# Optimization experiments

Hardware: AMD Instinct MI355X
Metric: run time of the kernel (lower is better)

Reference implementation:

```python
import jax, jax.numpy as jnp
import numpy as np

SEQ = 4096
R_DIM = 1024
Z_DIM = 1024
AT_DIM = 1024
G_DIM = 1024


def _xavier(key, shape):
    fan_in, fan_out = shape[1], shape[0]
    limit = float(np.sqrt(6.0 / (fan_in + fan_out)))
    return jax.random.uniform(key, shape, jnp.float32, -limit, limit)


def setup_inputs() -> dict:
    key = jax.random.key(0)
    ks = jax.random.split(key, 12)
    return {
        "R": jax.random.normal(ks[0], (SEQ, R_DIM), jnp.float32),
        "W_alpha": _xavier(ks[1], (R_DIM, 2 * R_DIM)),
        "b_alpha": jnp.zeros((R_DIM,), jnp.float32),
        "W_delta": _xavier(ks[2], (R_DIM, 2 * R_DIM)),
        "b_delta": jnp.zeros((R_DIM,), jnp.float32),
        "W_q": _xavier(ks[3], (AT_DIM, Z_DIM)),
        "b_q": jnp.zeros((AT_DIM,), jnp.float32),
        "W_k": _xavier(ks[4], (AT_DIM, Z_DIM)),
        "b_k": jnp.zeros((AT_DIM,), jnp.float32),
        "W_v": _xavier(ks[5], (AT_DIM, Z_DIM)),
        "b_v": jnp.zeros((AT_DIM,), jnp.float32),
        "W_z": _xavier(ks[6], (Z_DIM, R_DIM)),
        "b_z": jnp.zeros((Z_DIM,), jnp.float32),
        "W_f": _xavier(ks[7], (AT_DIM, G_DIM)),
        "b_f": jnp.zeros((AT_DIM,), jnp.float32),
        "W_EMA": _xavier(ks[8], (G_DIM, R_DIM)),
        "b_EMA": jnp.zeros((G_DIM,), jnp.float32),
        "W_z_at": _xavier(ks[9], (G_DIM, AT_DIM)),
        "b_z_at": jnp.zeros((G_DIM,), jnp.float32),
        "W_i": _xavier(ks[10], (1, R_DIM)),
        "b_i": jnp.zeros((1,), jnp.float32),
        "W_final": _xavier(ks[11], (1, G_DIM)),
    }


def reference(R, W_alpha, b_alpha, W_delta, b_delta, W_q, b_q, W_k, b_k,
              W_v, b_v, W_z, b_z, W_f, b_f, W_EMA, b_EMA, W_z_at, b_z_at,
              W_i, b_i, W_final):
    r_dim = R.shape[-1]
    at_dim = W_q.shape[0]
    # prepend zero row; r_t / r_{t-1} pairs
    R2 = jnp.concatenate([jnp.zeros((1, r_dim), R.dtype), R], axis=0)
    r_t, r_prev = R2[1:], R2[:-1]
    concat_r = jnp.concatenate([r_prev, r_t], axis=1)  # [m, 2r]
    alpha = jnp.tanh(concat_r @ W_alpha.T + b_alpha)
    delta = jnp.tanh(concat_r @ W_delta.T + b_delta)
    R_EMA = alpha * r_t + (1.0 - alpha) * delta * r_prev
    Z = jax.nn.silu(R_EMA @ W_z.T + b_z)
    Q = Z @ W_q.T + b_q
    K = Z @ W_k.T + b_k
    V = Z @ W_v.T + b_v
    scores = (Q @ K.T) / jnp.sqrt(jnp.float32(at_dim))  # [m, m]
    weights = jax.nn.softmax(scores, axis=-1)
    Z_at = weights @ V
    R_EMA_p = R_EMA @ W_EMA.T + b_EMA
    f = jax.nn.sigmoid(R_EMA_p @ W_f.T + b_f)
    Z_at_p = f * Z_at
    Z_EMA_f = Z_at_p @ W_z_at.T + b_z_at
    Z_tp = jnp.tanh(R_EMA_p + Z_EMA_f)
    i = jnp.tanh(R_EMA @ W_i.T + b_i)  # [m, 1]
    Z_final = i * Z_tp + (1.0 - i) * R_EMA_p
    p_hat = jax.nn.sigmoid(Z_final @ W_final.T)  # [m, 1]
    return p_hat
```

## Files before the change

kernel.cpp:

```cpp
#include <hip/hip_runtime.h>
#include <cstdint>
#include <cmath>

#define MB (1024ull * 1024ull)

typedef unsigned short u16;
typedef __attribute__((ext_vector_type(8))) short short8;
typedef __attribute__((ext_vector_type(4))) float f32x4;

enum { M_TANH = 0, M_ZRE = 1, M_QKVF = 2, M_SCALE = 3, M_PVRAW = 4, M_F32 = 5 };

__device__ __forceinline__ u16 f2b(float f) {
  union { float f; uint32_t u; } v; v.f = f;
  uint32_t r = v.u + 0x7FFFu + ((v.u >> 16) & 1u);
  return (u16)(r >> 16);
}
__device__ __forceinline__ float b2f(u16 u) {
  union { uint32_t u; float f; } v; v.u = ((uint32_t)u) << 16;
  return v.f;
}

typedef __attribute__((address_space(3))) uint32_t lds_u32;
typedef const __attribute__((address_space(1))) uint32_t glb_u32;

__device__ __forceinline__ void gload16(const void* g, void* l) {
  __builtin_amdgcn_global_load_lds((glb_u32*)g, (lds_u32*)l, 16, 0, 0);
}

template <int MODE, int BNT>
__global__ __launch_bounds__(256) void gemm(const u16* __restrict__ A,
                                            const u16* __restrict__ B,
                                            const float* __restrict__ bias,
                                            const u16* __restrict__ A2,
                                            const u16* __restrict__ B2,
                                            const float* __restrict__ bias2,
                                            u16* __restrict__ Cb,
                                            u16* __restrict__ Cb2,
                                            u16* __restrict__ Cb3,
                                            float* __restrict__ Cf,
                                            int K, int lda, int ldb, float scale) {
  constexpr int NI = 4;
  constexpr int NJ = (BNT == 128) ? 4 : 2;
  __shared__ u16 As[2][128 * 32];
  __shared__ u16 Bs[2][BNT * 32];
  const int tid = threadIdx.x;
  const int wid = tid >> 6, lane = tid & 63;

  const int gx = gridDim.x, nwg = gx * gridDim.y;
  int id = blockIdx.y * gx + blockIdx.x;
  if ((nwg & 7) == 0) id = (id & 7) * (nwg >> 3) + (id >> 3);
  const int bm = (id / gx) * 128, bn = (id % gx) * BNT;
  const int wm = wid >> 1, wn = wid & 1;
  const int rowbase = wm * 64, colbase = wn * (BNT / 2);

  const bool isf = (MODE == M_QKVF) && (bn >= 3072);
  const u16* Ab = isf ? A2 : A;
  const u16* Bb = isf ? B2 : B;
  const int bnl = isf ? bn - 3072 : bn;
  const int kofs = (MODE == M_PVRAW) ? (int)blockIdx.z * K : 0;

  const int srow = tid >> 2;
  const int schunk = (tid & 3) ^ ((srow >> 1) & 3);
  const u16* gA = Ab + (size_t)(bm + srow) * lda + kofs + schunk * 8;
  const u16* gB = Bb + (size_t)(bnl + srow) * ldb + kofs + schunk * 8;

  f32x4 acc[NI][NJ];
#pragma unroll
  for (int i = 0; i < NI; ++i)
#pragma unroll
    for (int j = 0; j < NJ; ++j) acc[i][j] = (f32x4){0.f, 0.f, 0.f, 0.f};

  const int ar = lane & 15;
  const int pch = (((lane >> 4) ^ ((ar >> 1) & 3))) * 8;

  const int NT = K >> 5;

  auto stage = [&](int buf, int t) {
    const u16* a = gA + (size_t)t * 32;
    const u16* b = gB + (size_t)t * 32;
    gload16(a, &As[buf][wid * 512]);
    gload16(a + (size_t)64 * lda, &As[buf][wid * 512 + 2048]);
    gload16(b, &Bs[buf][wid * 512]);
    if (BNT == 128) gload16(b + (size_t)64 * ldb, &Bs[buf][wid * 512 + 2048]);
  };

  stage(0, 0);
  __syncthreads();
  int cur = 0;
  for (int t = 0; t < NT; ++t) {
    if (t + 1 < NT) stage(cur ^ 1, t + 1);
    short8 af[NI], bf[NJ];
#pragma unroll
    for (int i = 0; i < NI; ++i)
      af[i] = *reinterpret_cast<const short8*>(&As[cur][(rowbase + i * 16 + ar) * 32 + pch]);
#pragma unroll
    for (int j = 0; j < NJ; ++j)
      bf[j] = *reinterpret_cast<const short8*>(&Bs[cur][(colbase + j * 16 + ar) * 32 + pch]);
    __builtin_amdgcn_s_setprio(1);
#pragma unroll
    for (int i = 0; i < NI; ++i)
#pragma unroll
      for (int j = 0; j < NJ; ++j)
        acc[i][j] = __builtin_amdgcn_mfma_f32_16x16x32_bf16(af[i], bf[j], acc[i][j], 0, 0, 0);
    __builtin_amdgcn_s_setprio(0);
    __syncthreads();
    cur ^= 1;
  }

  float* Cfz = Cf;
  if (MODE == M_PVRAW && blockIdx.z != 0) Cfz = (float*)Cb3;

#pragma unroll
  for (int i = 0; i < NI; ++i) {
    const int rb = bm + rowbase + i * 16 + (lane >> 4) * 4;
#pragma unroll
    for (int j = 0; j < NJ; ++j) {
      const int n = bn + colbase + j * 16 + (lane & 15);
#pragma unroll
      for (int r = 0; r < 4; ++r) {
        const int m = rb + r;
        float v = acc[i][j][r];
        if (MODE == M_TANH) {
          v = tanhf(v + bias[n]);
          Cb[(size_t)m * 2048 + n] = f2b(v);
        } else if (MODE == M_ZRE) {
          v += bias[n];
          if (n < 1024) { const float s = v / (1.f + expf(-v)); Cb[(size_t)m * 1024 + n] = f2b(s); }
          else Cb2[(size_t)m * 1024 + (n - 1024)] = f2b(v);
        } else if (MODE == M_QKVF) {
          if (isf) {
            const int nl = n - 3072;
            const float s = 1.f / (1.f + expf(-(v + bias2[nl])));
            Cb3[(size_t)m * 1024 + nl] = f2b(s);
          } else {
            v += bias[n];
            if (n < 2048) Cb[(size_t)m * 2048 + n] = f2b(v);
            else Cb2[(size_t)m * 1024 + (n - 2048)] = f2b(v);
          }
        } else if (MODE == M_SCALE) {
          Cb[(size_t)m * 4096 + n] = f2b(v * scale);
        } else if (MODE == M_PVRAW) {
          Cfz[(size_t)m * 1024 + n] = v;
        } else if (MODE == M_F32) {
          Cf[(size_t)m * 1024 + n] = v + bias[n];
        }
      }
    }
  }
}

__global__ __launch_bounds__(256) void pv_reduce(const float* __restrict__ p0,
                                                 const float* __restrict__ p1,
                                                 const u16* __restrict__ fvb,
                                                 u16* __restrict__ Zatp) {
  const int idx = blockIdx.x * 256 + threadIdx.x;
  const float4 a = reinterpret_cast<const float4*>(p0)[idx];
  const float4 b = reinterpret_cast<const float4*>(p1)[idx];
  const ushort4 f4 = reinterpret_cast<const ushort4*>(fvb)[idx];
  ushort4 o;
  o.x = f2b((a.x + b.x) * b2f(f4.x));
  o.y = f2b((a.y + b.y) * b2f(f4.y));
  o.z = f2b((a.z + b.z) * b2f(f4.z));
  o.w = f2b((a.w + b.w) * b2f(f4.w));
  reinterpret_cast<ushort4*>(Zatp)[idx] = o;
}

__global__ __launch_bounds__(256) void convert_all(
    const float* __restrict__ s0, const float* __restrict__ s1, const float* __restrict__ s2,
    const float* __restrict__ s3, const float* __restrict__ s4, const float* __restrict__ s5,
    const float* __restrict__ s6, const float* __restrict__ s7, const float* __restrict__ s8,
    u16* __restrict__ Wad, u16* __restrict__ Wze, u16* __restrict__ Wqkv,
    u16* __restrict__ Wfb, u16* __restrict__ Wzab) {
  const int idx = blockIdx.x * 256 + threadIdx.x;
  const float* src; u16* dst; int off;
  if      (idx < 524288)  { src = s0; dst = Wad;           off = idx; }
  else if (idx < 1048576) { src = s1; dst = Wad + 2097152; off = idx - 524288; }
  else if (idx < 1310720) { src = s2; dst = Wze;           off = idx - 1048576; }
  else if (idx < 1572864) { src = s3; dst = Wze + 1048576; off = idx - 1310720; }
  else if (idx < 1835008) { src = s4; dst = Wqkv;          off = idx - 1572864; }
  else if (idx < 2097152) { src = s5; dst = Wqkv + 1048576; off = idx - 1835008; }
  else if (idx < 2359296) { src = s6; dst = Wqkv + 2097152; off = idx - 2097152; }
  else if (idx < 2621440) { src = s7; dst = Wfb;           off = idx - 2359296; }
  else                    { src = s8; dst = Wzab;          off = idx - 2621440; }
  const float4 v = reinterpret_cast<const float4*>(src)[off];
  ushort4 o; o.x = f2b(v.x); o.y = f2b(v.y); o.z = f2b(v.z); o.w = f2b(v.w);
  reinterpret_cast<ushort4*>(dst)[off] = o;
}

__global__ void copy_bias(const float* __restrict__ ba, const float* __restrict__ bd,
                          const float* __restrict__ bz, const float* __restrict__ be,
                          const float* __restrict__ bq, const float* __restrict__ bk,
                          const float* __restrict__ bv,
                          float* __restrict__ bad, float* __restrict__ bze,
                          float* __restrict__ bqkv) {
  const int t = threadIdx.x;
  const float4* src; float4* dst;
  switch (blockIdx.x) {
    case 0: src = (const float4*)ba; dst = (float4*)bad; break;
    case 1: src = (const float4*)bd; dst = (float4*)(bad + 1024); break;
    case 2: src = (const float4*)bz; dst = (float4*)bze; break;
    case 3: src = (const float4*)be; dst = (float4*)(bze + 1024); break;
    case 4: src = (const float4*)bq; dst = (float4*)bqkv; break;
    case 5: src = (const float4*)bk; dst = (float4*)(bqkv + 1024); break;
    default: src = (const float4*)bv; dst = (float4*)(bqkv + 2048); break;
  }
  dst[t] = src[t];
}

__global__ __launch_bounds__(256) void concat_kern(const float* __restrict__ R,
                                                   u16* __restrict__ Rc) {
  const int idx = blockIdx.x * 256 + threadIdx.x;
  const int m = idx >> 9;
  const int c = (idx & 511) * 4;
  float4 v;
  if (c < 1024) {
    if (m > 0) v = *reinterpret_cast<const float4*>(&R[(size_t)(m - 1) * 1024 + c]);
    else v = make_float4(0.f, 0.f, 0.f, 0.f);
  } else {
    v = *reinterpret_cast<const float4*>(&R[(size_t)m * 1024 + (c - 1024)]);
  }
  ushort4 o; o.x = f2b(v.x); o.y = f2b(v.y); o.z = f2b(v.z); o.w = f2b(v.w);
  reinterpret_cast<ushort4*>(Rc)[idx] = o;
}

__global__ __launch_bounds__(256) void ema_combine(const float* __restrict__ R,
                                                   const u16* __restrict__ adb,
                                                   u16* __restrict__ REMA) {
  const int idx = blockIdx.x * 256 + threadIdx.x;
  const int m = idx >> 8, c4 = idx & 255;
  const float4 rt = reinterpret_cast<const float4*>(R)[idx];
  float4 rp = make_float4(0.f, 0.f, 0.f, 0.f);
  if (m > 0) rp = reinterpret_cast<const float4*>(R)[idx - 256];
  const ushort4 a4 = reinterpret_cast<const ushort4*>(adb)[m * 512 + c4];
  const ushort4 d4 = reinterpret_cast<const ushort4*>(adb)[m * 512 + 256 + c4];
  ushort4 o;
  { const float av = b2f(a4.x); o.x = f2b(av * rt.x + (1.f - av) * b2f(d4.x) * rp.x); }
  { const float av = b2f(a4.y); o.y = f2b(av * rt.y + (1.f - av) * b2f(d4.y) * rp.y); }
  { const float av = b2f(a4.z); o.z = f2b(av * rt.z + (1.f - av) * b2f(d4.z) * rp.z); }
  { const float av = b2f(a4.w); o.w = f2b(av * rt.w + (1.f - av) * b2f(d4.w) * rp.w); }
  reinterpret_cast<ushort4*>(REMA)[idx] = o;
}

__device__ __forceinline__ float waveMax(float v) {
#pragma unroll
  for (int o = 32; o; o >>= 1) v = fmaxf(v, __shfl_down(v, o));
  return v;
}
__device__ __forceinline__ float waveSum(float v) {
#pragma unroll
  for (int o = 32; o; o >>= 1) v += __shfl_down(v, o);
  return v;
}

__global__ __launch_bounds__(256) void softmax_rows(u16* __restrict__ S) {
  u16* p = S + (size_t)blockIdx.x * 4096;
  const int tid = threadIdx.x;
  float v[16];
#pragma unroll
  for (int j = 0; j < 4; ++j) {
    const ushort4 t = *reinterpret_cast<const ushort4*>(&p[tid * 4 + 1024 * j]);
    v[4 * j + 0] = b2f(t.x); v[4 * j + 1] = b2f(t.y);
    v[4 * j + 2] = b2f(t.z); v[4 * j + 3] = b2f(t.w);
  }
  float mx = -INFINITY;
#pragma unroll
  for (int j = 0; j < 16; ++j) mx = fmaxf(mx, v[j]);
  __shared__ float red[4];
  const float wm = waveMax(mx);
  if ((tid & 63) == 0) red[tid >> 6] = wm;
  __syncthreads();
  mx = fmaxf(fmaxf(red[0], red[1]), fmaxf(red[2], red[3]));
  __syncthreads();
  float sum = 0.f;
#pragma unroll
  for (int j = 0; j < 16; ++j) { v[j] = expf(v[j] - mx); sum += v[j]; }
  const float ws_ = waveSum(sum);
  if ((tid & 63) == 0) red[tid >> 6] = ws_;
  __syncthreads();
  const float inv = 1.f / (red[0] + red[1] + red[2] + red[3]);
#pragma unroll
  for (int j = 0; j < 4; ++j) {
    ushort4 t;
    t.x = f2b(v[4 * j + 0] * inv); t.y = f2b(v[4 * j + 1] * inv);
    t.z = f2b(v[4 * j + 2] * inv); t.w = f2b(v[4 * j + 3] * inv);
    *reinterpret_cast<ushort4*>(&p[tid * 4 + 1024 * j]) = t;
  }
}

__global__ __launch_bounds__(256) void transpose_b16(const u16* __restrict__ V,
                                                     u16* __restrict__ Vt) {
  __shared__ u16 t[64][72];
  const int bn = blockIdx.x * 64;
  const int bk = blockIdx.y * 64;
  const int tx = threadIdx.x & 15, ty = threadIdx.x >> 4;
#pragma unroll
  for (int i = 0; i < 64; i += 16) {
    const ushort4 v = *reinterpret_cast<const ushort4*>(&V[(size_t)(bk + ty + i) * 1024 + bn + tx * 4]);
    t[ty + i][tx * 4 + 0] = v.x; t[ty + i][tx * 4 + 1] = v.y;
    t[ty + i][tx * 4 + 2] = v.z; t[ty + i][tx * 4 + 3] = v.w;
  }
  __syncthreads();
#pragma unroll
  for (int i = 0; i < 64; i += 16) {
    ushort4 w;
    w.x = t[tx * 4 + 0][ty + i]; w.y = t[tx * 4 + 1][ty + i];
    w.z = t[tx * 4 + 2][ty + i]; w.w = t[tx * 4 + 3][ty + i];
    *reinterpret_cast<ushort4*>(&Vt[(size_t)(bn + ty + i) * 4096 + bk + tx * 4]) = w;
  }
}

__global__ void final_kern(const u16* __restrict__ REMAb, const u16* __restrict__ REMApb,
                           const float* __restrict__ ZEMAf,
                           const float* __restrict__ Wi, const float* __restrict__ bi,
                           const float* __restrict__ Wfin, float* __restrict__ out) {
  const int m = blockIdx.x, l = threadIdx.x;
  float si = 0.f;
#pragma unroll
  for (int j = 0; j < 16; ++j) {
    const int n = l + 64 * j;
    si += b2f(REMAb[(size_t)m * 1024 + n]) * Wi[n];
  }
#pragma unroll
  for (int o = 32; o; o >>= 1) si += __shfl_xor(si, o);
  const float im = tanhf(si + bi[0]);
  float s = 0.f;
#pragma unroll
  for (int j = 0; j < 16; ++j) {
    const int n = l + 64 * j;
    const float rp = b2f(REMApb[(size_t)m * 1024 + n]);
    const float zf = im * tanhf(rp + ZEMAf[(size_t)m * 1024 + n]) + (1.f - im) * rp;
    s += zf * Wfin[n];
  }
#pragma unroll
  for (int o = 32; o; o >>= 1) s += __shfl_down(s, o);
  if (l == 0) out[m] = 1.f / (1.f + expf(-s));
}

extern "C" void kernel_launch(void* const* d_in, const int* in_sizes, int n_in,
                              void* d_out, int out_size, void* d_ws, size_t ws_size,
                              hipStream_t stream) {
  const float* R       = (const float*)d_in[0];
  const float* W_alpha = (const float*)d_in[1];  const float* b_alpha = (const float*)d_in[2];
  const float* W_delta = (const float*)d_in[3];  const float* b_delta = (const float*)d_in[4];
  const float* W_q     = (const float*)d_in[5];  const float* b_q     = (const float*)d_in[6];
  const float* W_k     = (const float*)d_in[7];  const float* b_k     = (const float*)d_in[8];
  const float* W_v     = (const float*)d_in[9];  const float* b_v     = (const float*)d_in[10];
  const float* W_z     = (const float*)d_in[11]; const float* b_z     = (const float*)d_in[12];
  const float* W_f     = (const float*)d_in[13]; const float* b_f     = (const float*)d_in[14];
  const float* W_EMA   = (const float*)d_in[15]; const float* b_EMA   = (const float*)d_in[16];
  const float* W_z_at  = (const float*)d_in[17]; const float* b_z_at  = (const float*)d_in[18];
  const float* W_i     = (const float*)d_in[19]; const float* b_i     = (const float*)d_in[20];
  const float* W_final = (const float*)d_in[21];
  float* out = (float*)d_out;
  uint8_t* w8 = (uint8_t*)d_ws;

  u16*   Rc     = (u16*)(w8 + 0 * MB);
  u16*   Zb     = (u16*)(w8 + 0 * MB);
  u16*   Zatpb  = (u16*)(w8 + 0 * MB);
  u16*   REMApb = (u16*)(w8 + 8 * MB);
  u16*   Wad    = (u16*)(w8 + 16 * MB);
  u16*   fvb    = (u16*)(w8 + 16 * MB);
  u16*   adb    = (u16*)(w8 + 24 * MB);
  float* pvp0   = (float*)(w8 + 24 * MB);
  float* ZEMAf  = (float*)(w8 + 24 * MB);
  u16*   Wqkv   = (u16*)(w8 + 40 * MB);
  u16*   Vtb    = (u16*)(w8 + 40 * MB);
  u16*   Wze    = (u16*)(w8 + 46 * MB);
  u16*   Wfb    = (u16*)(w8 + 50 * MB);
  u16*   Wzab   = (u16*)(w8 + 52 * MB);
  u16*   REMAb  = (u16*)(w8 + 54 * MB);
  u16*   QKb    = (u16*)(w8 + 62 * MB);
  float* pvp1   = (float*)(w8 + 62 * MB);
  u16*   Vb     = (u16*)(w8 + 78 * MB);
  u16*   Sb     = (u16*)(w8 + 78 * MB);
  float* bad    = (float*)(w8 + 110 * MB + 64 * 1024);
  float* bze    = bad + 2048;
  float* bqkv   = bze + 2048;

  const dim3 blk(256);
  convert_all<<<11264, blk, 0, stream>>>(W_alpha, W_delta, W_z, W_EMA, W_q, W_k, W_v, W_f, W_z_at,
                                         Wad, Wze, Wqkv, Wfb, Wzab);
  concat_kern<<<8192, blk, 0, stream>>>(R, Rc);
  copy_bias<<<7, blk, 0, stream>>>(b_alpha, b_delta, b_z, b_EMA, b_q, b_k, b_v, bad, bze, bqkv);

  gemm<M_TANH, 128><<<dim3(16, 32), blk, 0, stream>>>(
      Rc, Wad, bad, nullptr, nullptr, nullptr, adb, nullptr, nullptr, nullptr, 2048, 2048, 2048, 1.f);
  ema_combine<<<4096, blk, 0, stream>>>(R, adb, REMAb);
  gemm<M_ZRE, 128><<<dim3(16, 32), blk, 0, stream>>>(
      REMAb, Wze, bze, nullptr, nullptr, nullptr, Zb, REMApb, nullptr, nullptr, 1024, 1024, 1024, 1.f);
  gemm<M_QKVF, 128><<<dim3(32, 32), blk, 0, stream>>>(
      Zb, Wqkv, bqkv, REMApb, Wfb, b_f, QKb, Vb, fvb, nullptr, 1024, 1024, 1024, 1.f);
  transpose_b16<<<dim3(16, 64), blk, 0, stream>>>(Vb, Vtb);
  gemm<M_SCALE, 128><<<dim3(32, 32), blk, 0, stream>>>(
      QKb, QKb + 1024, nullptr, nullptr, nullptr, nullptr, Sb, nullptr, nullptr, nullptr, 1024, 2048, 2048, 0.03125f);
  softmax_rows<<<4096, blk, 0, stream>>>(Sb);
  gemm<M_PVRAW, 128><<<dim3(8, 32, 2), blk, 0, stream>>>(
      Sb, Vtb, nullptr, nullptr, nullptr, nullptr, nullptr, nullptr, (u16*)pvp1, pvp0, 2048, 4096, 4096, 1.f);
  pv_reduce<<<4096, blk, 0, stream>>>(pvp0, pvp1, fvb, Zatpb);
  gemm<M_F32, 64><<<dim3(16, 32), blk, 0, stream>>>(
      Zatpb, Wzab, b_z_at, nullptr, nullptr, nullptr, nullptr, nullptr, nullptr, ZEMAf, 1024, 1024, 1024, 1.f);
  final_kern<<<4096, 64, 0, stream>>>(REMAb, REMApb, ZEMAf, W_i, b_i, W_final, out);
}
```

Measured before the change: 355.4 us.

## Replace 128-wide GEMMs with 256x256 8-wave ping-pong pipelined kernel

Introduces gemm8, a 512-thread kernel that computes 256x256 output tiles with K-step 64 and an XOR-swizzled LDS layout. The main loop interleaves LDS fragment reads, async global-to-LDS loads for the next K tiles, and MFMA quadrants separated by explicit barriers and vmcnt waits, overlapping memory with compute. All large GEMMs except the final F32 projection now use it, with grids shrunk to match. The larger tiles raise reuse of each loaded element but use 128KB of LDS per block and many registers, and launch fewer workgroups, which can leave CUs underused on the smaller GEMMs.

```diff
diff --git a/kernel.cpp b/kernel.cpp
--- a/kernel.cpp
+++ b/kernel.cpp
@@ -27,31 +27,31 @@
   __builtin_amdgcn_global_load_lds((glb_u32*)g, (lds_u32*)l, 16, 0, 0);
 }
 
-template <int MODE, int BNT>
-__global__ __launch_bounds__(256) void gemm(const u16* __restrict__ A,
-                                            const u16* __restrict__ B,
-                                            const float* __restrict__ bias,
-                                            const u16* __restrict__ A2,
-                                            const u16* __restrict__ B2,
-                                            const float* __restrict__ bias2,
-                                            u16* __restrict__ Cb,
-                                            u16* __restrict__ Cb2,
-                                            u16* __restrict__ Cb3,
-                                            float* __restrict__ Cf,
-                                            int K, int lda, int ldb, float scale) {
-  constexpr int NI = 4;
-  constexpr int NJ = (BNT == 128) ? 4 : 2;
-  __shared__ u16 As[2][128 * 32];
-  __shared__ u16 Bs[2][BNT * 32];
+#define SBAR asm volatile("s_barrier" ::: "memory")
+
+template <int MODE>
+__global__ __launch_bounds__(512, 2) void gemm8(const u16* __restrict__ A,
+                                                const u16* __restrict__ B,
+                                                const float* __restrict__ bias,
+                                                const u16* __restrict__ A2,
+                                                const u16* __restrict__ B2,
+                                                const float* __restrict__ bias2,
+                                                u16* __restrict__ Cb,
+                                                u16* __restrict__ Cb2,
+                                                u16* __restrict__ Cb3,
+                                                float* __restrict__ Cf,
+                                                int K, int lda, int ldb, float scale) {
+  __shared__ u16 As[2][256 * 64];
+  __shared__ u16 Bs[2][256 * 64];
   const int tid = threadIdx.x;
   const int wid = tid >> 6, lane = tid & 63;
+  const int wr = wid >> 2, wc = wid & 3;
+  const int ar = lane & 15;
 
   const int gx = gridDim.x, nwg = gx * gridDim.y;
   int id = blockIdx.y * gx + blockIdx.x;
   if ((nwg & 7) == 0) id = (id & 7) * (nwg >> 3) + (id >> 3);
-  const int bm = (id / gx) * 128, bn = (id % gx) * BNT;
-  const int wm = wid >> 1, wn = wid & 1;
-  const int rowbase = wm * 64, colbase = wn * (BNT / 2);
+  const int bm = (id / gx) * 256, bn = (id % gx) * 256;
 
   const bool isf = (MODE == M_QKVF) && (bn >= 3072);
   const u16* Ab = isf ? A2 : A;
@@ -59,67 +59,122 @@
   const int bnl = isf ? bn - 3072 : bn;
   const int kofs = (MODE == M_PVRAW) ? (int)blockIdx.z * K : 0;
 
-  const int srow = tid >> 2;
-  const int schunk = (tid & 3) ^ ((srow >> 1) & 3);
-  const u16* gA = Ab + (size_t)(bm + srow) * lda + kofs + schunk * 8;
-  const u16* gB = Bb + (size_t)(bnl + srow) * ldb + kofs + schunk * 8;
-
-  f32x4 acc[NI][NJ];
-#pragma unroll
-  for (int i = 0; i < NI; ++i)
-#pragma unroll
-    for (int j = 0; j < NJ; ++j) acc[i][j] = (f32x4){0.f, 0.f, 0.f, 0.f};
-
-  const int ar = lane & 15;
-  const int pch = (((lane >> 4) ^ ((ar >> 1) & 3))) * 8;
-
-  const int NT = K >> 5;
-
-  auto stage = [&](int buf, int t) {
-    const u16* a = gA + (size_t)t * 32;
-    const u16* b = gB + (size_t)t * 32;
-    gload16(a, &As[buf][wid * 512]);
-    gload16(a + (size_t)64 * lda, &As[buf][wid * 512 + 2048]);
-    gload16(b, &Bs[buf][wid * 512]);
-    if (BNT == 128) gload16(b + (size_t)64 * ldb, &Bs[buf][wid * 512 + 2048]);
+  const int NKT = K >> 6;
+
+  auto stA = [&](int slot, int half, int kt) {
+    if (kt >= NKT) return;
+#pragma unroll
+    for (int l = 0; l < 2; ++l) {
+      const int grow = half * 128 + l * 64 + (tid >> 3);
+      const u16* src = Ab + (size_t)(bm + grow) * lda + kofs + kt * 64 +
+                       (((tid & 7) ^ (grow & 7)) << 3);
+      gload16(src, &As[slot][(half * 128 + l * 64) * 64 + tid * 8]);
+    }
   };
-
-  stage(0, 0);
-  __syncthreads();
-  int cur = 0;
-  for (int t = 0; t < NT; ++t) {
-    if (t + 1 < NT) stage(cur ^ 1, t + 1);
-    short8 af[NI], bf[NJ];
-#pragma unroll
-    for (int i = 0; i < NI; ++i)
-      af[i] = *reinterpret_cast<const short8*>(&As[cur][(rowbase + i * 16 + ar) * 32 + pch]);
-#pragma unroll
-    for (int j = 0; j < NJ; ++j)
-      bf[j] = *reinterpret_cast<const short8*>(&Bs[cur][(colbase + j * 16 + ar) * 32 + pch]);
+  auto stB = [&](int slot, int half, int kt) {
+    if (kt >= NKT) return;
+#pragma unroll
+    for (int l = 0; l < 2; ++l) {
+      const int grow = half * 128 + l * 64 + (tid >> 3);
+      const u16* src = Bb + (size_t)(bnl + grow) * ldb + kofs + kt * 64 +
+                       (((tid & 7) ^ (grow & 7)) << 3);
+      gload16(src, &Bs[slot][(half * 128 + l * 64) * 64 + tid * 8]);
+    }
+  };
+
+  f32x4 acc[8][4];
+#pragma unroll
+  for (int i = 0; i < 8; ++i)
+#pragma unroll
+    for (int j = 0; j < 4; ++j) acc[i][j] = (f32x4){0.f, 0.f, 0.f, 0.f};
+
+  short8 Ar[4][2], B0r[2][2], B1r[2][2];
+
+  auto rdA4 = [&](int slot, int rbase) {
+#pragma unroll
+    for (int rg = 0; rg < 4; ++rg)
+#pragma unroll
+      for (int kk = 0; kk < 2; ++kk) {
+        const int row = wr * 128 + rbase + rg * 16 + ar;
+        const int kc = kk * 4 + (lane >> 4);
+        Ar[rg][kk] = *reinterpret_cast<const short8*>(
+            &As[slot][row * 64 + ((kc ^ (row & 7)) << 3)]);
+      }
+  };
+  auto rdB2 = [&](int slot, int cbase, short8 (&Br)[2][2]) {
+#pragma unroll
+    for (int cg = 0; cg < 2; ++cg)
+#pragma unroll
+      for (int kk = 0; kk < 2; ++kk) {
+        const int row = wc * 64 + cbase + cg * 16 + ar;
+        const int kc = kk * 4 + (lane >> 4);
+        Br[cg][kk] = *reinterpret_cast<const short8*>(
+            &Bs[slot][row * 64 + ((kc ^ (row & 7)) << 3)]);
+      }
+  };
+  auto quad = [&](int qr, int qc, short8 (&Br)[2][2]) {
     __builtin_amdgcn_s_setprio(1);
 #pragma unroll
-    for (int i = 0; i < NI; ++i)
-#pragma unroll
-      for (int j = 0; j < NJ; ++j)
-        acc[i][j] = __builtin_amdgcn_mfma_f32_16x16x32_bf16(af[i], bf[j], acc[i][j], 0, 0, 0);
+    for (int rg = 0; rg < 4; ++rg)
+#pragma unroll
+      for (int cg = 0; cg < 2; ++cg)
+#pragma unroll
+        for (int kk = 0; kk < 2; ++kk)
+          acc[qr * 4 + rg][qc * 2 + cg] = __builtin_amdgcn_mfma_f32_16x16x32_bf16(
+              Ar[rg][kk], Br[cg][kk], acc[qr * 4 + rg][qc * 2 + cg], 0, 0, 0);
     __builtin_amdgcn_s_setprio(0);
-    __syncthreads();
-    cur ^= 1;
+  };
+
+  stA(0, 0, 0); stA(0, 1, 0); stB(0, 0, 0); stB(0, 1, 0);
+  stB(1, 0, 1); stB(1, 1, 1);
+  asm volatile("s_waitcnt vmcnt(4)" ::: "memory");
+  SBAR;
+
+  const int NIT = NKT >> 1;
+  for (int i = 0; i < NIT; ++i) {
+    const int kt1 = 2 * i + 1, kt2a = 2 * i + 2, kt2b = 2 * i + 3;
+    const bool last = (i + 1 == NIT);
+    rdA4(0, 0); rdB2(0, 0, B0r);
+    stA(1, 0, kt1);
+    SBAR; quad(0, 0, B0r); SBAR;
+    rdB2(0, 32, B1r);
+    stA(1, 1, kt1);
+    SBAR; quad(0, 1, B1r); SBAR;
+    rdA4(0, 64);
+    stB(0, 0, kt2a);
+    SBAR; quad(1, 1, B1r); SBAR;
+    stB(0, 1, kt2a);
+    if (last) asm volatile("s_waitcnt vmcnt(0)" ::: "memory");
+    else      asm volatile("s_waitcnt vmcnt(4)" ::: "memory");
+    SBAR; quad(1, 0, B0r); SBAR;
+    rdA4(1, 0); rdB2(1, 0, B0r);
+    stA(0, 0, kt2a);
+    SBAR; quad(0, 0, B0r); SBAR;
+    rdB2(1, 32, B1r);
+    stA(0, 1, kt2a);
+    SBAR; quad(0, 1, B1r); SBAR;
+    rdA4(1, 64);
+    stB(1, 0, kt2b);
+    SBAR; quad(1, 1, B1r); SBAR;
+    stB(1, 1, kt2b);
+    if (last) asm volatile("s_waitcnt vmcnt(0)" ::: "memory");
+    else      asm volatile("s_waitcnt vmcnt(4)" ::: "memory");
+    SBAR; quad(1, 0, B0r); SBAR;
   }
 
   float* Cfz = Cf;
   if (MODE == M_PVRAW && blockIdx.z != 0) Cfz = (float*)Cb3;
 
 #pragma unroll
-  for (int i = 0; i < NI; ++i) {
-    const int rb = bm + rowbase + i * 16 + (lane >> 4) * 4;
-#pragma unroll
-    for (int j = 0; j < NJ; ++j) {
-      const int n = bn + colbase + j * 16 + (lane & 15);
+  for (int ii = 0; ii < 8; ++ii) {
+    const int rb = bm + wr * 128 + ii * 16 + (lane >> 4) * 4;
+#pragma unroll
+    for (int j = 0; j < 4; ++j) {
+      const int n = bn + wc * 64 + j * 16 + ar;
 #pragma unroll
       for (int r = 0; r < 4; ++r) {
         const int m = rb + r;
-        float v = acc[i][j][r];
+        float v = acc[ii][j][r];
         if (MODE == M_TANH) {
           v = tanhf(v + bias[n]);
           Cb[(size_t)m * 2048 + n] = f2b(v);
@@ -141,9 +196,81 @@
           Cb[(size_t)m * 4096 + n] = f2b(v * scale);
         } else if (MODE == M_PVRAW) {
           Cfz[(size_t)m * 1024 + n] = v;
-        } else if (MODE == M_F32) {
-          Cf[(size_t)m * 1024 + n] = v + bias[n];
         }
+      }
+    }
+  }
+}
+
+template <int MODE, int BNT>
+__global__ __launch_bounds__(256) void gemm(const u16* __restrict__ A,
+                                            const u16* __restrict__ B,
+                                            const float* __restrict__ bias,
+                                            u16* __restrict__ Cb,
+                                            float* __restrict__ Cf,
+                                            int K, int lda, int ldb) {
+  constexpr int NI = 4;
+  constexpr int NJ = (BNT == 128) ? 4 : 2;
+  __shared__ u16 As[2][128 * 32];
+  __shared__ u16 Bs[2][BNT * 32];
+  const int tid = threadIdx.x;
+  const int wid = tid >> 6, lane = tid & 63;
+  const int gx = gridDim.x, nwg = gx * gridDim.y;
+  int id = blockIdx.y * gx + blockIdx.x;
+  if ((nwg & 7) == 0) id = (id & 7) * (nwg >> 3) + (id >> 3);
+  const int bm = (id / gx) * 128, bn = (id % gx) * BNT;
+  const int wm = wid >> 1, wn = wid & 1;
+  const int rowbase = wm * 64, colbase = wn * (BNT / 2);
+  const int srow = tid >> 2;
+  const int schunk = (tid & 3) ^ ((srow >> 1) & 3);
+  const u16* gA = A + (size_t)(bm + srow) * lda + schunk * 8;
+  const u16* gB = B + (size_t)(bn + srow) * ldb + schunk * 8;
+  f32x4 acc[NI][NJ];
+#pragma unroll
+  for (int i = 0; i < NI; ++i)
+#pragma unroll
+    for (int j = 0; j < NJ; ++j) acc[i][j] = (f32x4){0.f, 0.f, 0.f, 0.f};
+  const int ar = lane & 15;
+  const int pch = (((lane >> 4) ^ ((ar >> 1) & 3))) * 8;
+  const int NT = K >> 5;
+  auto stage = [&](int buf, int t) {
+    const u16* a = gA + (size_t)t * 32;
+    const u16* b = gB + (size_t)t * 32;
+    gload16(a, &As[buf][wid * 512]);
+    gload16(a + (size_t)64 * lda, &As[buf][wid * 512 + 2048]);
+    gload16(b, &Bs[buf][wid * 512]);
+    if (BNT == 128) gload16(b + (size_t)64 * ldb, &Bs[buf][wid * 512 + 2048]);
+  };
+  stage(0, 0);
+  __syncthreads();
+  int cur = 0;
+  for (int t = 0; t < NT; ++t) {
+    if (t + 1 < NT) stage(cur ^ 1, t + 1);
+    short8 af[NI], bf[NJ];
+#pragma unroll
+    for (int i = 0; i < NI; ++i)
+      af[i] = *reinterpret_cast<const short8*>(&As[cur][(rowbase + i * 16 + ar) * 32 + pch]);
+#pragma unroll
+    for (int j = 0; j < NJ; ++j)
+      bf[j] = *reinterpret_cast<const short8*>(&Bs[cur][(colbase + j * 16 + ar) * 32 + pch]);
+#pragma unroll
+    for (int i = 0; i < NI; ++i)
+#pragma unroll
+      for (int j = 0; j < NJ; ++j)
+        acc[i][j] = __builtin_amdgcn_mfma_f32_16x16x32_bf16(af[i], bf[j], acc[i][j], 0, 0, 0);
+    __syncthreads();
+    cur ^= 1;
+  }
+#pragma unroll
+  for (int i = 0; i < NI; ++i) {
+    const int rb = bm + rowbase + i * 16 + (lane >> 4) * 4;
+#pragma unroll
+    for (int j = 0; j < NJ; ++j) {
+      const int n = bn + colbase + j * 16 + (lane & 15);
+#pragma unroll
+      for (int r = 0; r < 4; ++r) {
+        const int m = rb + r;
+        if (MODE == M_F32) Cf[(size_t)m * 1024 + n] = acc[i][j][r] + bias[n];
       }
     }
   }
@@ -383,21 +510,21 @@
   concat_kern<<<8192, blk, 0, stream>>>(R, Rc);
   copy_bias<<<7, blk, 0, stream>>>(b_alpha, b_delta, b_z, b_EMA, b_q, b_k, b_v, bad, bze, bqkv);
 
-  gemm<M_TANH, 128><<<dim3(16, 32), blk, 0, stream>>>(
+  gemm8<M_TANH><<<dim3(8, 16), 512, 0, stream>>>(
       Rc, Wad, bad, nullptr, nullptr, nullptr, adb, nullptr, nullptr, nullptr, 2048, 2048, 2048, 1.f);
   ema_combine<<<4096, blk, 0, stream>>>(R, adb, REMAb);
-  gemm<M_ZRE, 128><<<dim3(16, 32), blk, 0, stream>>>(
+  gemm8<M_ZRE><<<dim3(8, 16), 512, 0, stream>>>(
       REMAb, Wze, bze, nullptr, nullptr, nullptr, Zb, REMApb, nullptr, nullptr, 1024, 1024, 1024, 1.f);
-  gemm<M_QKVF, 128><<<dim3(32, 32), blk, 0, stream>>>(
+  gemm8<M_QKVF><<<dim3(16, 16), 512, 0, stream>>>(
       Zb, Wqkv, bqkv, REMApb, Wfb, b_f, QKb, Vb, fvb, nullptr, 1024, 1024, 1024, 1.f);
   transpose_b16<<<dim3(16, 64), blk, 0, stream>>>(Vb, Vtb);
-  gemm<M_SCALE, 128><<<dim3(32, 32), blk, 0, stream>>>(
+  gemm8<M_SCALE><<<dim3(16, 16), 512, 0, stream>>>(
       QKb, QKb + 1024, nullptr, nullptr, nullptr, nullptr, Sb, nullptr, nullptr, nullptr, 1024, 2048, 2048, 0.03125f);
   softmax_rows<<<4096, blk, 0, stream>>>(Sb);
-  gemm<M_PVRAW, 128><<<dim3(8, 32, 2), blk, 0, stream>>>(
+  gemm8<M_PVRAW><<<dim3(4, 16, 2), 512, 0, stream>>>(
       Sb, Vtb, nullptr, nullptr, nullptr, nullptr, nullptr, nullptr, (u16*)pvp1, pvp0, 2048, 4096, 4096, 1.f);
   pv_reduce<<<4096, blk, 0, stream>>>(pvp0, pvp1, fvb, Zatpb);
   gemm<M_F32, 64><<<dim3(16, 32), blk, 0, stream>>>(
-      Zatpb, Wzab, b_z_at, nullptr, nullptr, nullptr, nullptr, nullptr, nullptr, ZEMAf, 1024, 1024, 1024, 1.f);
+      Zatpb, Wzab, b_z_at, nullptr, ZEMAf, 1024, 1024, 1024);
   final_kern<<<4096, 64, 0, stream>>>(REMAb, REMApb, ZEMAf, W_i, b_i, W_final, out);
 }
```

New measurement: 365.8 us. 2.9% more time.
